# Optimization experiments

Hardware: AMD Instinct MI355X
Metric: run time of the kernel (lower is better)

Reference implementation:

```python
import jax, jax.numpy as jnp
import numpy as np

R, C = 9, 9  # local window (rows, cols)


def setup_inputs() -> dict:
    key = jax.random.key(0)
    k1, k2, k3, k4, k5 = jax.random.split(key, 5)
    q = jax.random.normal(k1, (8, 256, 128, 128), jnp.float32)      # (B, q_size, H, W)
    c_t = jax.random.normal(k2, (8, 256, 512), jnp.float32)          # (B, T, c_size)
    W_a = jax.random.normal(k3, (512, 256), jnp.float32) * 0.04      # Linear(q_size -> c_size), no bias
    W_p = jax.random.normal(k4, (256, 512), jnp.float32) * 0.04      # Linear(c_size -> p_size)
    V_p = jax.random.normal(k5, (2, 256), jnp.float32) * 0.06        # Linear(p_size -> 2)
    return {"q": q, "c_t": c_t, "W_a": W_a, "W_p": W_p, "V_p": V_p}


def reference(q, c_t, W_a, W_p, V_p):
    B, D, H, W = q.shape
    T = c_t.shape[1]
    S = H  # q.size(2) before padding

    # predictive alignment: p_t = S * sigmoid(V_p(tanh(W_p(c_t))))  -> (B, T, 2)
    p_t = S * jax.nn.sigmoid(jnp.tanh(c_t @ W_p.T) @ V_p.T)

    # pad top/left with NaN, flatten spatial dims
    qp = jnp.pad(q, ((0, 0), (0, 0), (1, 0), (1, 0)), constant_values=jnp.nan)
    rows, cols = H + 1, W + 1
    qf = qp.reshape(B, D, rows * cols).transpose(0, 2, 1)  # (B, rows*cols, D)

    roff = jnp.arange(-(R // 2), (R + 1) // 2)  # R offsets
    coff = jnp.arange(-(C // 2), (C + 1) // 2)  # C offsets
    r = jnp.clip(jnp.round(p_t[..., 0]).astype(jnp.int32)[..., None] + roff + 1, 0, rows) % rows  # (B,T,R)
    c = jnp.clip(jnp.round(p_t[..., 1]).astype(jnp.int32)[..., None] + coff + 1, 0, cols) % cols  # (B,T,C)

    # flat window indices, order i*C + j (matches torch stack order)
    s = (r[..., :, None] * cols + c[..., None, :]).reshape(B, T, R * C)

    # gather windows: (B, T, R*C, D)
    qg = jnp.take_along_axis(qf, s.reshape(B, T * R * C, 1), axis=1).reshape(B, T, R * C, D)
    nan_loc = jnp.isnan(qg[..., 0])                    # (B, T, R*C)
    qg = jnp.where(nan_loc[..., None], 0.0, qg)

    # Gaussian positional weighting
    rexp = -2.0 * ((jnp.clip(r - 1, 0, None).astype(jnp.float32) - p_t[..., 0:1]) / (R // 2)) ** 2
    cexp = -2.0 * ((jnp.clip(c - 1, 0, None).astype(jnp.float32) - p_t[..., 1:2]) / (C // 2)) ** 2
    gauss = jnp.exp((rexp[..., :, None] + cexp[..., None, :]).reshape(B, T, R * C))

    # score: (W_a q) . c_t  -> (B, T, R*C)
    a_t = jnp.einsum('btkd,cd,btc->btk', qg, W_a, c_t)
    a_t = jnp.where(nan_loc, -jnp.inf, a_t)
    W_attn = jax.nn.softmax(a_t, axis=2) * gauss

    out = jnp.einsum('btk,btkd->btd', W_attn, qg)  # (B, T, D)
    return out
```

## Files before the change

kernel.cpp:

```cpp
#include <hip/hip_runtime.h>
#include <math.h>

#define Bq 8
#define Tt 256
#define Dd 256
#define Hh 128
#define Ww 128
#define Cc 512
#define HW (Hh*Ww)
#define NBT (Bq*Tt)

__device__ __forceinline__ float lane_bcast(float x, int l) {
    return __uint_as_float(__builtin_amdgcn_readlane(__float_as_uint(x), l));
}

__global__ __launch_bounds__(256) void transpose_wp(
    const float* __restrict__ W_p, float* __restrict__ WpT)
{
    __shared__ float tile[32][33];
    const int bx = blockIdx.x;
    const int by = blockIdx.y;
    const int lx = threadIdx.x & 31, ly = threadIdx.x >> 5;
#pragma unroll
    for (int j = 0; j < 4; j++) {
        int p = by * 32 + ly + j * 8;
        tile[ly + j * 8][lx] = W_p[(size_t)p * Cc + bx * 32 + lx];
    }
    __syncthreads();
#pragma unroll
    for (int j = 0; j < 4; j++) {
        int c = bx * 32 + ly + j * 8;
        WpT[(size_t)c * 256 + by * 32 + lx] = tile[lx][ly + j * 8];
    }
}

#define TOK 8
__global__ __launch_bounds__(512) void prep_kernel(
    const float* __restrict__ c_t,
    const float* __restrict__ W_a,
    const float* __restrict__ WpT,
    const float* __restrict__ V_p,
    float* __restrict__ u_ws,
    float* __restrict__ p_ws)
{
    __shared__ float y0s[TOK][256];
    __shared__ float y1s[TOK][256];
    const int tid  = threadIdx.x;
    const int o    = tid & 255;
    const int half = tid >> 8;
    const int ln   = tid & 63;
    const int bt0  = blockIdx.x * TOK;

    const float* Wcol = (half ? WpT : W_a) + o;
    const float* ctb  = c_t + (size_t)bt0 * Cc;

    float acc[TOK];
#pragma unroll
    for (int t = 0; t < TOK; t++) acc[t] = 0.f;

    float ctr[TOK], ctn[TOK];
#pragma unroll
    for (int t = 0; t < TOK; t++) ctr[t] = ctb[t * Cc + ln];

#pragma unroll
    for (int c0 = 0; c0 < Cc; c0 += 64) {
        if (c0 + 64 < Cc) {
#pragma unroll
            for (int t = 0; t < TOK; t++) ctn[t] = ctb[t * Cc + c0 + 64 + ln];
        }
#pragma unroll
        for (int cc8 = 0; cc8 < 64; cc8 += 8) {
            float w[8];
#pragma unroll
            for (int j = 0; j < 8; j++)
                w[j] = Wcol[(size_t)(c0 + cc8 + j) * 256];
#pragma unroll
            for (int j = 0; j < 8; j++) {
#pragma unroll
                for (int t = 0; t < TOK; t++)
                    acc[t] = fmaf(lane_bcast(ctr[t], cc8 + j), w[j], acc[t]);
            }
        }
#pragma unroll
        for (int t = 0; t < TOK; t++) ctr[t] = ctn[t];
    }

    if (half == 0) {
#pragma unroll
        for (int t = 0; t < TOK; t++)
            u_ws[(size_t)(bt0 + t) * Dd + o] = acc[t];
    } else {
        float v0 = V_p[o], v1 = V_p[256 + o];
#pragma unroll
        for (int t = 0; t < TOK; t++) {
            float th = tanhf(acc[t]);
            y0s[t][o] = th * v0;
            y1s[t][o] = th * v1;
        }
    }
    __syncthreads();

    const int wv = tid >> 6;
    float s0 = y0s[wv][ln] + y0s[wv][ln + 64] + y0s[wv][ln + 128] + y0s[wv][ln + 192];
    float s1 = y1s[wv][ln] + y1s[wv][ln + 64] + y1s[wv][ln + 128] + y1s[wv][ln + 192];
#pragma unroll
    for (int of = 32; of >= 1; of >>= 1) {
        s0 += __shfl_xor(s0, of);
        s1 += __shfl_xor(s1, of);
    }
    if (ln == 0) {
        p_ws[(size_t)(bt0 + wv) * 2 + 0] = 128.f / (1.f + expf(-s0));
        p_ws[(size_t)(bt0 + wv) * 2 + 1] = 128.f / (1.f + expf(-s1));
    }
}

__global__ __launch_bounds__(256) void attn_kernel(
    const float* __restrict__ q,
    const float* __restrict__ u_ws,
    const float* __restrict__ p_ws,
    float* __restrict__ out)
{
    __shared__ __align__(16) _Float16 win[Dd][9][12];
    __shared__ __align__(16) float pacc_s[8][9][12];
    __shared__ float ascore[9][12];
    __shared__ float u_s[Dd];
    __shared__ float w_s[81];
    __shared__ float a_s[81];
    __shared__ float e_s[81];
    __shared__ float rex_s[9], cex_s[9];
    __shared__ int   rr_s[9], cc_s[9];
    __shared__ float m_sh, inv_sh;

    const int tid = threadIdx.x;
    int bt = blockIdx.x;
    bt = ((bt & 7) << 8) | (bt >> 3);
    const int b = bt >> 8;

    u_s[tid] = u_ws[(size_t)bt * Dd + tid];

    if (tid < 18) {
        int   i = (tid < 9) ? tid : tid - 9;
        float p = p_ws[(size_t)bt * 2 + ((tid < 9) ? 0 : 1)];
        int base = (int)rintf(p);
        int v = base + i - 3;
        v = min(max(v, 0), 129) % 129;
        float cl = (float)max(v - 1, 0);
        float z  = (cl - p) * 0.25f;
        float ex = -2.f * z * z;
        if (tid < 9) { rr_s[i] = v; rex_s[i] = ex; }
        else         { cc_s[i] = v; cex_s[i] = ex; }
    }
    __syncthreads();

    int jc0 = 0, c0 = 1;
#pragma unroll
    for (int j = 8; j >= 0; j--)
        if (cc_s[j] > 0) { jc0 = j; c0 = cc_s[j]; }
    const int cb = min((c0 - 1) & ~3, Ww - 12);
    const int e0 = (c0 - 1) - cb;

    {
        const int g  = tid >> 5;
        const int l5 = tid & 31;
        const bool lact = (l5 < 27);
        const int li = lact ? ((l5 * 171) >> 9) : 0;
        const int lv = l5 - li * 3;
        const int vr = lact ? rr_s[li] : 1;
        const int rowoff = (max(vr, 1) - 1) * Ww + cb + 4 * lv;
        const float* qp = q + (size_t)b * Dd * HW + rowoff;

        if (lact) {
            float u_r[32];
#pragma unroll
            for (int m = 0; m < 32; m++) u_r[m] = u_s[g + 8 * m];

            float px = 0.f, py = 0.f, pz = 0.f, pw = 0.f;
            float4 xb[2][4];
#pragma unroll
            for (int mm = 0; mm < 4; mm++)
                xb[0][mm] = *(const float4*)(qp + (size_t)(g + 8 * mm) * HW);

            for (int it = 0; it < 8; it++) {
                const int cur = it & 1;
                if (it < 7) {
#pragma unroll
                    for (int mm = 0; mm < 4; mm++)
                        xb[cur ^ 1][mm] = *(const float4*)
                            (qp + (size_t)(g + 8 * (4 * (it + 1) + mm)) * HW);
                }
#pragma unroll
                for (int mm = 0; mm < 4; mm++) {
                    const int m  = 4 * it + mm;
                    const int d0 = g + 8 * m;
                    float4 x = xb[cur][mm];
                    float  u = u_r[m];
                    px = fmaf(x.x, u, px); py = fmaf(x.y, u, py);
                    pz = fmaf(x.z, u, pz); pw = fmaf(x.w, u, pw);
                    union { _Float16 h[4]; uint2 uu; } pk;
                    pk.h[0] = (_Float16)x.x; pk.h[1] = (_Float16)x.y;
                    pk.h[2] = (_Float16)x.z; pk.h[3] = (_Float16)x.w;
                    *(uint2*)&win[d0][li][4 * lv] = pk.uu;
                }
            }
            *(float4*)&pacc_s[g][li][4 * lv] = make_float4(px, py, pz, pw);
        }
    }
    __syncthreads();

    if (tid < 108) {
        const int li  = tid / 12;
        const int pos = tid - li * 12;
        float s = 0.f;
#pragma unroll
        for (int g = 0; g < 8; g++) s += pacc_s[g][li][pos];
        ascore[li][pos] = s;
    }
    __syncthreads();

    float a_val = -INFINITY;
    bool  valid_k = false;
    if (tid < 81) {
        const int ki = (tid * 57) >> 9;
        const int kj = tid - ki * 9;
        valid_k = (rr_s[ki] > 0) && (cc_s[kj] > 0);
        const int pos = min(max(e0 + kj - jc0, 0), 11);
        a_val = valid_k ? ascore[ki][pos] : -INFINITY;
        a_s[tid] = a_val;
    }
    __syncthreads();

    if (tid < 64) {
        float m = a_s[tid];
        if (tid + 64 < 81) m = fmaxf(m, a_s[tid + 64]);
        for (int o = 32; o >= 1; o >>= 1) m = fmaxf(m, __shfl_xor(m, o));
        if (tid == 0) m_sh = m;
    }
    __syncthreads();
    {
        float e = 0.f;
        if (tid < 81 && valid_k) e = expf(a_val - m_sh);
        if (tid < 81) e_s[tid] = e;
    }
    __syncthreads();
    if (tid < 64) {
        float sv = e_s[tid] + ((tid + 64 < 81) ? e_s[tid + 64] : 0.f);
        for (int o = 32; o >= 1; o >>= 1) sv += __shfl_xor(sv, o);
        if (tid == 0) inv_sh = 1.f / sv;
    }
    __syncthreads();
    if (tid < 81) {
        int i = (tid * 57) >> 9;
        int j = tid - i * 9;
        float g = expf(rex_s[i] + cex_s[j]);
        w_s[tid] = e_s[tid] * inv_sh * g;
    }
    __syncthreads();

    int posj[9];
#pragma unroll
    for (int j = 0; j < 9; j++) posj[j] = min(max(e0 + j - jc0, 0), 11);
    const _Float16* wd = &win[tid][0][0];
    float acc = 0.f;
#pragma unroll
    for (int k = 0; k < 81; k++) {
        const int ki = k / 9, kj = k % 9;
        acc = fmaf(w_s[k], (float)wd[ki * 12 + posj[kj]], acc);
    }
    out[(size_t)bt * Dd + tid] = acc;
}

extern "C" void kernel_launch(void* const* d_in, const int* in_sizes, int n_in,
                              void* d_out, int out_size, void* d_ws, size_t ws_size,
                              hipStream_t stream) {
    const float* q   = (const float*)d_in[0];
    const float* c_t = (const float*)d_in[1];
    const float* W_a = (const float*)d_in[2];
    const float* W_p = (const float*)d_in[3];
    const float* V_p = (const float*)d_in[4];
    float* out  = (float*)d_out;
    float* u_ws = (float*)d_ws;
    float* p_ws = u_ws + (size_t)NBT * Dd;
    float* WpT  = p_ws + (size_t)NBT * 2;

    transpose_wp<<<dim3(16, 8), 256, 0, stream>>>(W_p, WpT);
    prep_kernel<<<NBT / TOK, 512, 0, stream>>>(c_t, W_a, WpT, V_p, u_ws, p_ws);
    attn_kernel<<<NBT, 256, 0, stream>>>(q, u_ws, p_ws, out);
}
```

Baseline: 263.2 us.

## Keep gathered window in registers and reduce output via wave shuffles

The attention kernel now launches 512 threads per block, and each thread loads 16 float4 window chunks up front and keeps them in registers. This replaces the fp16 shared-memory window copy and the per-d 81-tap loop. Weights are scattered into a padded 9x12 position grid, and the output for each d is formed by a shuffle reduction across lanes, then staged through shared memory. This removes the large LDS window buffer and its fp16 conversion, and issues all global loads at once. The cost is higher register pressure and many cross-lane shuffles.

```diff
diff --git a/kernel.cpp b/kernel.cpp
--- a/kernel.cpp
+++ b/kernel.cpp
@@ -114,17 +114,16 @@
     }
 }
 
-__global__ __launch_bounds__(256) void attn_kernel(
+__global__ __launch_bounds__(512, 4) void attn_kernel(
     const float* __restrict__ q,
     const float* __restrict__ u_ws,
     const float* __restrict__ p_ws,
     float* __restrict__ out)
 {
-    __shared__ __align__(16) _Float16 win[Dd][9][12];
-    __shared__ __align__(16) float pacc_s[8][9][12];
-    __shared__ float ascore[9][12];
+    __shared__ __align__(16) float pacc_s[16][9][12];
+    __shared__ __align__(16) float wpos[9][12];
     __shared__ float u_s[Dd];
-    __shared__ float w_s[81];
+    __shared__ float out_s[Dd];
     __shared__ float a_s[81];
     __shared__ float e_s[81];
     __shared__ float rex_s[9], cex_s[9];
@@ -136,7 +135,8 @@
     bt = ((bt & 7) << 8) | (bt >> 3);
     const int b = bt >> 8;
 
-    u_s[tid] = u_ws[(size_t)bt * Dd + tid];
+    if (tid < Dd) u_s[tid] = u_ws[(size_t)bt * Dd + tid];
+    if (tid < 81) a_s[tid] = -INFINITY;
 
     if (tid < 18) {
         int   i = (tid < 9) ? tid : tid - 9;
@@ -159,73 +159,41 @@
     const int cb = min((c0 - 1) & ~3, Ww - 12);
     const int e0 = (c0 - 1) - cb;
 
-    {
-        const int g  = tid >> 5;
-        const int l5 = tid & 31;
-        const bool lact = (l5 < 27);
-        const int li = lact ? ((l5 * 171) >> 9) : 0;
-        const int lv = l5 - li * 3;
-        const int vr = lact ? rr_s[li] : 1;
+    const int g  = tid >> 5;
+    const int l5 = tid & 31;
+    const bool lact = (l5 < 27);
+    const int li = lact ? ((l5 * 171) >> 9) : 0;
+    const int lv = l5 - li * 3;
+
+    float4 xb[16];
+    if (lact) {
+        const int vr = rr_s[li];
         const int rowoff = (max(vr, 1) - 1) * Ww + cb + 4 * lv;
         const float* qp = q + (size_t)b * Dd * HW + rowoff;
-
-        if (lact) {
-            float u_r[32];
-#pragma unroll
-            for (int m = 0; m < 32; m++) u_r[m] = u_s[g + 8 * m];
-
-            float px = 0.f, py = 0.f, pz = 0.f, pw = 0.f;
-            float4 xb[2][4];
-#pragma unroll
-            for (int mm = 0; mm < 4; mm++)
-                xb[0][mm] = *(const float4*)(qp + (size_t)(g + 8 * mm) * HW);
-
-            for (int it = 0; it < 8; it++) {
-                const int cur = it & 1;
-                if (it < 7) {
-#pragma unroll
-                    for (int mm = 0; mm < 4; mm++)
-                        xb[cur ^ 1][mm] = *(const float4*)
-                            (qp + (size_t)(g + 8 * (4 * (it + 1) + mm)) * HW);
-                }
-#pragma unroll
-                for (int mm = 0; mm < 4; mm++) {
-                    const int m  = 4 * it + mm;
-                    const int d0 = g + 8 * m;
-                    float4 x = xb[cur][mm];
-                    float  u = u_r[m];
-                    px = fmaf(x.x, u, px); py = fmaf(x.y, u, py);
-                    pz = fmaf(x.z, u, pz); pw = fmaf(x.w, u, pw);
-                    union { _Float16 h[4]; uint2 uu; } pk;
-                    pk.h[0] = (_Float16)x.x; pk.h[1] = (_Float16)x.y;
-                    pk.h[2] = (_Float16)x.z; pk.h[3] = (_Float16)x.w;
-                    *(uint2*)&win[d0][li][4 * lv] = pk.uu;
-                }
-            }
-            *(float4*)&pacc_s[g][li][4 * lv] = make_float4(px, py, pz, pw);
-        }
+#pragma unroll
+        for (int m = 0; m < 16; m++)
+            xb[m] = *(const float4*)(qp + (size_t)(g + 16 * m) * HW);
+
+        float px = 0.f, py = 0.f, pz = 0.f, pw = 0.f;
+#pragma unroll
+        for (int m = 0; m < 16; m++) {
+            const float u = u_s[g + 16 * m];
+            px = fmaf(xb[m].x, u, px); py = fmaf(xb[m].y, u, py);
+            pz = fmaf(xb[m].z, u, pz); pw = fmaf(xb[m].w, u, pw);
+        }
+        *(float4*)&pacc_s[g][li][4 * lv] = make_float4(px, py, pz, pw);
     }
     __syncthreads();
 
     if (tid < 108) {
-        const int li  = tid / 12;
-        const int pos = tid - li * 12;
+        const int lii = tid / 12;
+        const int pos = tid - lii * 12;
         float s = 0.f;
 #pragma unroll
-        for (int g = 0; g < 8; g++) s += pacc_s[g][li][pos];
-        ascore[li][pos] = s;
-    }
-    __syncthreads();
-
-    float a_val = -INFINITY;
-    bool  valid_k = false;
-    if (tid < 81) {
-        const int ki = (tid * 57) >> 9;
-        const int kj = tid - ki * 9;
-        valid_k = (rr_s[ki] > 0) && (cc_s[kj] > 0);
-        const int pos = min(max(e0 + kj - jc0, 0), 11);
-        a_val = valid_k ? ascore[ki][pos] : -INFINITY;
-        a_s[tid] = a_val;
+        for (int gg = 0; gg < 16; gg++) s += pacc_s[gg][lii][pos];
+        const int kj = pos - e0 + jc0;
+        if (kj >= 0 && kj < 9 && rr_s[lii] > 0 && cc_s[kj] > 0)
+            a_s[lii * 9 + kj] = s;
     }
     __syncthreads();
 
@@ -236,10 +204,9 @@
         if (tid == 0) m_sh = m;
     }
     __syncthreads();
-    {
-        float e = 0.f;
-        if (tid < 81 && valid_k) e = expf(a_val - m_sh);
-        if (tid < 81) e_s[tid] = e;
+    if (tid < 81) {
+        const float av = a_s[tid];
+        e_s[tid] = (av == -INFINITY) ? 0.f : expf(av - m_sh);
     }
     __syncthreads();
     if (tid < 64) {
@@ -248,25 +215,44 @@
         if (tid == 0) inv_sh = 1.f / sv;
     }
     __syncthreads();
-    if (tid < 81) {
-        int i = (tid * 57) >> 9;
-        int j = tid - i * 9;
-        float g = expf(rex_s[i] + cex_s[j]);
-        w_s[tid] = e_s[tid] * inv_sh * g;
-    }
-    __syncthreads();
-
-    int posj[9];
-#pragma unroll
-    for (int j = 0; j < 9; j++) posj[j] = min(max(e0 + j - jc0, 0), 11);
-    const _Float16* wd = &win[tid][0][0];
-    float acc = 0.f;
-#pragma unroll
-    for (int k = 0; k < 81; k++) {
-        const int ki = k / 9, kj = k % 9;
-        acc = fmaf(w_s[k], (float)wd[ki * 12 + posj[kj]], acc);
-    }
-    out[(size_t)bt * Dd + tid] = acc;
+
+    if (tid < 108) {
+        const int lii = tid / 12;
+        const int pos = tid - lii * 12;
+        const int kj  = pos - e0 + jc0;
+        float w = 0.f;
+        if (kj >= 0 && kj < 9 && rr_s[lii] > 0 && cc_s[kj] > 0)
+            w = e_s[lii * 9 + kj] * inv_sh * expf(rex_s[lii] + cex_s[kj]);
+        wpos[lii][pos] = w;
+    }
+    __syncthreads();
+
+    float po[16];
+    if (lact) {
+        const float4 wv = *(const float4*)&wpos[li][4 * lv];
+#pragma unroll
+        for (int m = 0; m < 16; m++) {
+            float acc = xb[m].x * wv.x;
+            acc = fmaf(xb[m].y, wv.y, acc);
+            acc = fmaf(xb[m].z, wv.z, acc);
+            acc = fmaf(xb[m].w, wv.w, acc);
+            po[m] = acc;
+        }
+    } else {
+#pragma unroll
+        for (int m = 0; m < 16; m++) po[m] = 0.f;
+    }
+#pragma unroll
+    for (int o = 16; o >= 1; o >>= 1) {
+#pragma unroll
+        for (int m = 0; m < 16; m++) po[m] += __shfl_xor(po[m], o);
+    }
+    if (l5 == 0) {
+#pragma unroll
+        for (int m = 0; m < 16; m++) out_s[g + 16 * m] = po[m];
+    }
+    __syncthreads();
+    if (tid < Dd) out[(size_t)bt * Dd + tid] = out_s[tid];
 }
 
 extern "C" void kernel_launch(void* const* d_in, const int* in_sizes, int n_in,
@@ -284,5 +270,5 @@
 
     transpose_wp<<<dim3(16, 8), 256, 0, stream>>>(W_p, WpT);
     prep_kernel<<<NBT / TOK, 512, 0, stream>>>(c_t, W_a, WpT, V_p, u_ws, p_ws);
-    attn_kernel<<<NBT, 256, 0, stream>>>(q, u_ws, p_ws, out);
-}
+    attn_kernel<<<NBT, 512, 0, stream>>>(q, u_ws, p_ws, out);
+}
```

New measurement: 387.8 us. 47.3% more time.
